# Optimization experiments

Hardware: AMD Instinct MI355X
Metric: run time of the kernel (lower is better)

Reference implementation:

```python
import jax, jax.numpy as jnp
import numpy as np

DIM = 1024
HEADS = 16
DIM_HEAD = 64
INNER = HEADS * DIM_HEAD
SCALE = DIM_HEAD ** -0.5
LN_EPS = 1e-5
MASK_VALUE = -np.finfo(np.float32).max


def setup_inputs() -> dict:
    key = jax.random.key(0)
    ks = jax.random.split(key, 3)
    x = jax.random.normal(ks[0], (2, 2048, DIM), dtype=jnp.float32)
    w_qkv = jax.random.normal(ks[1], (DIM, 3 * INNER), dtype=jnp.float32) * (DIM ** -0.5)
    w_out = jax.random.normal(ks[2], (INNER, DIM), dtype=jnp.float32) * (INNER ** -0.5)
    ln_gamma = jnp.ones((DIM,), dtype=jnp.float32)
    ln_beta = jnp.zeros((DIM,), dtype=jnp.float32)
    return {"x": x, "ln_gamma": ln_gamma, "ln_beta": ln_beta, "w_qkv": w_qkv, "w_out": w_out}


def reference(x, ln_gamma, ln_beta, w_qkv, w_out):
    b, n, _ = x.shape
    # LayerNorm
    mu = jnp.mean(x, axis=-1, keepdims=True)
    var = jnp.mean(jnp.square(x - mu), axis=-1, keepdims=True)
    xn = (x - mu) * jax.lax.rsqrt(var + LN_EPS) * ln_gamma + ln_beta
    # QKV projection, split into heads: b n (h d) -> b h n d
    qkv = xn @ w_qkv  # [b, n, 3*inner]
    q, k, v = jnp.split(qkv, 3, axis=-1)
    def to_heads(t):
        return t.reshape(b, n, HEADS, DIM_HEAD).transpose(0, 2, 1, 3)
    q, k, v = to_heads(q), to_heads(k), to_heads(v)
    # scaled scores with diagonal excluded
    dots = jnp.einsum('bhnd,bhmd->bhnm', q, k) * SCALE
    eye = jnp.eye(n, dtype=bool)
    dots = jnp.where(eye, MASK_VALUE, dots)
    attn = jax.nn.softmax(dots, axis=-1)
    out = jnp.einsum('bhnm,bhmd->bhnd', attn, v)
    out = out.transpose(0, 2, 1, 3).reshape(b, n, INNER)
    return out @ w_out
```

## Files before the change

### kernel.cpp

```cpp
#include <hip/hip_runtime.h>


#define DIMM   1024
#define NSEQ   2048
#define BATCH  2
#define HEADS  16
#define DHEAD  64
#define QKVN   3072
#define MROWS  4096

typedef float          f32x4  __attribute__((ext_vector_type(4)));
typedef __bf16         bf16x8 __attribute__((ext_vector_type(8)));
typedef __bf16         bf16x4 __attribute__((ext_vector_type(4)));
typedef unsigned short u16x8  __attribute__((ext_vector_type(8)));
typedef unsigned short u16x4  __attribute__((ext_vector_type(4)));

#define QSCALE (0.125f * 1.4426950408889634f)

#if __has_builtin(__builtin_amdgcn_exp2f)
#define EXP2(x) __builtin_amdgcn_exp2f(x)
#else
#define EXP2(x) exp2f(x)
#endif

__device__ __forceinline__ unsigned short f2bf(float f) {
  unsigned u = __builtin_bit_cast(unsigned, f);
  u += 0x7FFFu + ((u >> 16) & 1u);
  return (unsigned short)(u >> 16);
}
__device__ __forceinline__ bf16x8 as_bf(u16x8 v) { return __builtin_bit_cast(bf16x8, v); }

__device__ __forceinline__ u16x4 cvt4(f32x4 v) {
  bf16x4 b;
  b[0] = (__bf16)v[0]; b[1] = (__bf16)v[1]; b[2] = (__bf16)v[2]; b[3] = (__bf16)v[3];
  return __builtin_bit_cast(u16x4, b);
}

__device__ __forceinline__ void gl_lds16(const unsigned short* g, unsigned short* l) {
  __builtin_amdgcn_global_load_lds(
      (const __attribute__((address_space(1))) unsigned*)g,
      (__attribute__((address_space(3))) unsigned*)l, 16, 0, 0);
}

__device__ __forceinline__ bf16x8 lds_frag(const unsigned short* base, int row, int chunk) {
  return as_bf(*(const u16x8*)&base[row * 64 + ((chunk ^ (row & 7)) << 3)]);
}

__global__ __launch_bounds__(256) void transpose_bf16_kernel(
    const float* __restrict__ src, unsigned short* __restrict__ dst, int R, int C) {
  __shared__ float t[32][33];
  const int rb = blockIdx.y * 32, cb = blockIdx.x * 32;
  const int r0 = threadIdx.x >> 5;
  const int c  = threadIdx.x & 31;
#pragma unroll
  for (int i = 0; i < 4; ++i)
    t[r0 + i * 8][c] = src[(rb + r0 + i * 8) * C + cb + c];
  __syncthreads();
#pragma unroll
  for (int i = 0; i < 4; ++i)
    dst[(cb + r0 + i * 8) * R + rb + c] = f2bf(t[c][r0 + i * 8]);
}

__global__ __launch_bounds__(256) void ln_kernel(
    const float* __restrict__ x, const float* __restrict__ g,
    const float* __restrict__ be, unsigned short* __restrict__ xn) {
  const int row = blockIdx.x, tid = threadIdx.x;
  const int wave = tid >> 6, lane = tid & 63;
  const float4 v = *(const float4*)&x[row * DIMM + tid * 4];
  float s  = v.x + v.y + v.z + v.w;
  float s2 = v.x * v.x + v.y * v.y + v.z * v.z + v.w * v.w;
#pragma unroll
  for (int o = 32; o >= 1; o >>= 1) { s += __shfl_xor(s, o); s2 += __shfl_xor(s2, o); }
  __shared__ float ps[4], ps2[4];
  if (lane == 0) { ps[wave] = s; ps2[wave] = s2; }
  __syncthreads();
  s  = ps[0] + ps[1] + ps[2] + ps[3];
  s2 = ps2[0] + ps2[1] + ps2[2] + ps2[3];
  const float mu  = s * (1.0f / DIMM);
  const float var = s2 * (1.0f / DIMM) - mu * mu;
  const float rs  = rsqrtf(var + 1e-5f);
  const float4 gg = *(const float4*)&g[tid * 4];
  const float4 bb = *(const float4*)&be[tid * 4];
  u16x4 o;
  o[0] = f2bf((v.x - mu) * rs * gg.x + bb.x);
  o[1] = f2bf((v.y - mu) * rs * gg.y + bb.y);
  o[2] = f2bf((v.z - mu) * rs * gg.z + bb.z);
  o[3] = f2bf((v.w - mu) * rs * gg.w + bb.w);
  *(u16x4*)&xn[row * DIMM + tid * 4] = o;
}

template<bool SWAP>
__device__ __forceinline__ void gemm_core128(
    const unsigned short* __restrict__ A, const unsigned short* __restrict__ Bt,
    unsigned short* As, unsigned short* Bs, int bm, int bn, int tid,
    f32x4 (&acc)[4][4]) {
  const int wave = tid >> 6, lane = tid & 63;
  const int l15 = lane & 15, quad = lane >> 4;
  const int wm = wave >> 1, wn = wave & 1;
  const int lrow = lane >> 3;
  const int gcol = ((lane & 7) ^ lrow) << 3;
  const unsigned short* Ab = A  + (bm * 128 + wave * 32 + lrow) * DIMM + gcol;
  const unsigned short* Bb = Bt + (bn * 128 + wave * 32 + lrow) * DIMM + gcol;

  for (int k0 = 0; k0 < DIMM; k0 += 64) {
#pragma unroll
    for (int j = 0; j < 4; ++j) {
      gl_lds16(Ab + j * 8 * DIMM + k0, &As[(wave * 32 + j * 8) * 64]);
      gl_lds16(Bb + j * 8 * DIMM + k0, &Bs[(wave * 32 + j * 8) * 64]);
    }
    __syncthreads();
#pragma unroll
    for (int kk = 0; kk < 2; ++kk) {
      bf16x8 af[4], bfr[4];
#pragma unroll
      for (int mi = 0; mi < 4; ++mi) af[mi]  = lds_frag(As, wm * 64 + mi * 16 + l15, kk * 4 + quad);
#pragma unroll
      for (int ni = 0; ni < 4; ++ni) bfr[ni] = lds_frag(Bs, wn * 64 + ni * 16 + l15, kk * 4 + quad);
#pragma unroll
      for (int mi = 0; mi < 4; ++mi)
#pragma unroll
        for (int ni = 0; ni < 4; ++ni)
          acc[mi][ni] = SWAP
            ? __builtin_amdgcn_mfma_f32_16x16x32_bf16(bfr[ni], af[mi], acc[mi][ni], 0, 0, 0)
            : __builtin_amdgcn_mfma_f32_16x16x32_bf16(af[mi], bfr[ni], acc[mi][ni], 0, 0, 0);
    }
    __syncthreads();
  }
}

__global__ __launch_bounds__(256, 2) void gemm_qk_kernel(
    const unsigned short* __restrict__ A, const unsigned short* __restrict__ Bt,
    unsigned short* __restrict__ qb, unsigned short* __restrict__ kb) {
  __shared__ __attribute__((aligned(16))) unsigned short As[128 * 64];
  __shared__ __attribute__((aligned(16))) unsigned short Bs[128 * 64];
  const int tid = threadIdx.x;
  const int bm = blockIdx.y, bn = blockIdx.x;
  f32x4 acc[4][4] = {};
  gemm_core128<true>(A, Bt, As, Bs, bm, bn, tid, acc);

  const int lane = tid & 63, wave = tid >> 6;
  const int l15 = lane & 15, quad = lane >> 4;
  const int wm = wave >> 1, wn = wave & 1;
  const int colbase = bn * 128 + wn * 64;
  const int which = colbase >> 10;
  unsigned short* dst = which ? kb : qb;
  const float sc = which ? 1.0f : QSCALE;
#pragma unroll
  for (int mi = 0; mi < 4; ++mi) {
    const int m = bm * 128 + wm * 64 + mi * 16 + l15;
    const int bh0 = (m >> 11) * HEADS;
    const int n = m & 2047;
#pragma unroll
    for (int ni = 0; ni < 4; ++ni) {
      const int wc = (colbase & 1023) + ni * 16 + quad * 4;
      const int h = wc >> 6, dd = wc & 63;
      f32x4 v = acc[mi][ni] * sc;
      *(u16x4*)&dst[((bh0 + h) * NSEQ + n) * DHEAD + dd] = cvt4(v);
    }
  }
}

__global__ __launch_bounds__(256, 2) void gemm_v_kernel(
    const unsigned short* __restrict__ A, const unsigned short* __restrict__ Bt,
    unsigned short* __restrict__ vtb) {
  __shared__ __attribute__((aligned(16))) unsigned short As[128 * 64];
  __shared__ __attribute__((aligned(16))) unsigned short Bs[128 * 64];
  const int tid = threadIdx.x;
  const int bm = blockIdx.y, bn = blockIdx.x + 16;
  f32x4 acc[4][4] = {};
  gemm_core128<false>(A, Bt, As, Bs, bm, bn, tid, acc);

  const int lane = tid & 63, wave = tid >> 6;
  const int l15 = lane & 15, quad = lane >> 4;
  const int wm = wave >> 1, wn = wave & 1;
  const int colbase = bn * 128 + wn * 64 - 2048;
#pragma unroll
  for (int mi = 0; mi < 4; ++mi) {
    const int m0 = bm * 128 + wm * 64 + mi * 16 + quad * 4;
    const int bh0 = (m0 >> 11) * HEADS;
    const int n0 = m0 & 2047;
#pragma unroll
    for (int ni = 0; ni < 4; ++ni) {
      const int vcol = colbase + ni * 16 + l15;
      const int h = vcol >> 6, dd = vcol & 63;
      *(u16x4*)&vtb[((bh0 + h) * DHEAD + dd) * NSEQ + n0] = cvt4(acc[mi][ni]);
    }
  }
}

__global__ __launch_bounds__(256, 2) void attn_kernel(
    const unsigned short* __restrict__ qb, const unsigned short* __restrict__ kb,
    const unsigned short* __restrict__ vtb, unsigned short* __restrict__ attn_out) {
  __shared__ __attribute__((aligned(16))) unsigned short Ks[64 * 64];
  __shared__ __attribute__((aligned(16))) unsigned short Vts[64 * 64];
  __shared__ __attribute__((aligned(16))) unsigned short Ps[4][16][72];
  const int tid = threadIdx.x, wave = tid >> 6, lane = tid & 63;
  const int l15 = lane & 15, quad = lane >> 4;
  const int bh = blockIdx.x, qt = blockIdx.y;
  const int b = bh >> 4, h = bh & 15;
  const int qt64 = qt * 64;
  const int qg = qt64 + wave * 16 + l15;

  bf16x8 aq[2];
  const unsigned short* qrow = qb + (bh * NSEQ + qg) * DHEAD;
  aq[0] = as_bf(*(const u16x8*)(qrow + quad * 8));
  aq[1] = as_bf(*(const u16x8*)(qrow + 32 + quad * 8));

  float lsum = 0.f;
  f32x4 occ[4] = {};

  const int lrow = lane >> 3;
  const int gcol = ((lane & 7) ^ lrow) << 3;
  const unsigned short* Kb = kb  + (bh * NSEQ + wave * 16 + lrow) * DHEAD + gcol;
  const unsigned short* Vb = vtb + (bh * DHEAD + wave * 16 + lrow) * NSEQ + gcol;

  for (int kv = 0; kv < NSEQ; kv += 64) {
    gl_lds16(Kb + kv * DHEAD,             &Ks[(wave * 16) * 64]);
    gl_lds16(Kb + kv * DHEAD + 8 * DHEAD, &Ks[(wave * 16 + 8) * 64]);
    gl_lds16(Vb + kv,                     &Vts[(wave * 16) * 64]);
    gl_lds16(Vb + kv + 8 * NSEQ,          &Vts[(wave * 16 + 8) * 64]);
    __syncthreads();

    f32x4 scc[4];
#pragma unroll
    for (int ct = 0; ct < 4; ++ct) scc[ct] = (f32x4){-32.f, -32.f, -32.f, -32.f};
#pragma unroll
    for (int kk = 0; kk < 2; ++kk)
#pragma unroll
      for (int ct = 0; ct < 4; ++ct) {
        bf16x8 ak = lds_frag(Ks, ct * 16 + l15, kk * 4 + quad);
        scc[ct] = __builtin_amdgcn_mfma_f32_16x16x32_bf16(ak, aq[kk], scc[ct], 0, 0, 0);
      }

#pragma unroll
    for (int ct = 0; ct < 4; ++ct)
#pragma unroll
      for (int r = 0; r < 4; ++r) scc[ct][r] = EXP2(scc[ct][r]);

    if (kv == qt64) {
#pragma unroll
      for (int ct = 0; ct < 4; ++ct)
#pragma unroll
        for (int r = 0; r < 4; ++r) {
          const int kvo = ct * 16 + quad * 4 + r;
          if (kvo == wave * 16 + l15) scc[ct][r] = 0.f;
        }
    }

    f32x4 ps4 = (scc[0] + scc[1]) + (scc[2] + scc[3]);
    lsum += (ps4[0] + ps4[1]) + (ps4[2] + ps4[3]);

#pragma unroll
    for (int ct = 0; ct < 4; ++ct)
      *(u16x4*)&Ps[wave][l15][ct * 16 + quad * 4] = cvt4(scc[ct]);

#pragma unroll
    for (int kk = 0; kk < 2; ++kk) {
      bf16x8 bp = as_bf(*(const u16x8*)&Ps[wave][l15][kk * 32 + quad * 8]);
#pragma unroll
      for (int ct = 0; ct < 4; ++ct) {
        bf16x8 av = lds_frag(Vts, ct * 16 + l15, kk * 4 + quad);
        occ[ct] = __builtin_amdgcn_mfma_f32_16x16x32_bf16(av, bp, occ[ct], 0, 0, 0);
      }
    }
    __syncthreads();
  }
  lsum += __shfl_xor(lsum, 16);
  lsum += __shfl_xor(lsum, 32);
  const float rl = __builtin_amdgcn_rcpf(lsum);
#pragma unroll
  for (int ct = 0; ct < 4; ++ct) {
    f32x4 ov = occ[ct] * rl;
    *(u16x4*)&attn_out[(b * NSEQ + qg) * DIMM + h * DHEAD + ct * 16 + quad * 4] = cvt4(ov);
  }
}

__global__ __launch_bounds__(256, 2) void gemm_out_kernel(
    const unsigned short* __restrict__ A,
    const unsigned short* __restrict__ Bt,
    float* __restrict__ out) {
  __shared__ __attribute__((aligned(16))) unsigned short As[128 * 64];
  __shared__ __attribute__((aligned(16))) unsigned short Bs[128 * 64];
  const int tid = threadIdx.x;
  const int bm = blockIdx.y, bn = blockIdx.x;
  f32x4 acc[4][4] = {};
  gemm_core128<false>(A, Bt, As, Bs, bm, bn, tid, acc);

  const int lane = tid & 63, wave = tid >> 6;
  const int l15 = lane & 15, quad = lane >> 4;
  const int wm = wave >> 1, wn = wave & 1;
#pragma unroll
  for (int mi = 0; mi < 4; ++mi) {
    const int mrow = bm * 128 + wm * 64 + mi * 16 + quad * 4;
#pragma unroll
    for (int ni = 0; ni < 4; ++ni) {
      const int ncol = bn * 128 + wn * 64 + ni * 16 + l15;
#pragma unroll
      for (int r = 0; r < 4; ++r)
        out[(mrow + r) * DIMM + ncol] = acc[mi][ni][r];
    }
  }
}

extern "C" void kernel_launch(void* const* d_in, const int* in_sizes, int n_in,
                              void* d_out, int out_size, void* d_ws, size_t ws_size,
                              hipStream_t stream) {
  const float* x     = (const float*)d_in[0];
  const float* gamma = (const float*)d_in[1];
  const float* beta  = (const float*)d_in[2];
  const float* w_qkv = (const float*)d_in[3];
  const float* w_out = (const float*)d_in[4];
  float* out = (float*)d_out;

  char* ws = (char*)d_ws;
  unsigned short* xn    = (unsigned short*)(ws);
  unsigned short* wqkvT = (unsigned short*)(ws + 8388608);
  unsigned short* woutT = (unsigned short*)(ws + 14680064);
  unsigned short* qbuf  = (unsigned short*)(ws + 16777216);
  unsigned short* kbuf  = (unsigned short*)(ws + 25165824);
  unsigned short* vtbuf = (unsigned short*)(ws + 33554432);
  unsigned short* attnb = (unsigned short*)(ws + 41943040);

  transpose_bf16_kernel<<<dim3(QKVN / 32, DIMM / 32), 256, 0, stream>>>(w_qkv, wqkvT, DIMM, QKVN);
  transpose_bf16_kernel<<<dim3(DIMM / 32, DIMM / 32), 256, 0, stream>>>(w_out, woutT, DIMM, DIMM);
  ln_kernel<<<MROWS, 256, 0, stream>>>(x, gamma, beta, xn);
  gemm_qk_kernel<<<dim3(16, MROWS / 128), 256, 0, stream>>>(xn, wqkvT, qbuf, kbuf);
  gemm_v_kernel<<<dim3(8, MROWS / 128), 256, 0, stream>>>(xn, wqkvT, vtbuf);
  attn_kernel<<<dim3(BATCH * HEADS, NSEQ / 64), 256, 0, stream>>>(qbuf, kbuf, vtbuf, attnb);
  gemm_out_kernel<<<dim3(DIMM / 128, MROWS / 128), 256, 0, stream>>>(attnb, woutT, out);
}
```

Before: 203.2 us.

## Merge launches, double-buffer and widen attention q-tiles, vectorize output stores

The two weight transposes and the Q/K and V projection GEMMs are each merged into single launches, removing launch gaps and tail effects. The attention kernel now handles 128 queries per block (two 16-row subtiles per wave) and reuses each K/V fragment load across both. It also double-buffers the K/V tiles so the next tile's global-to-LDS copy overlaps compute. The output GEMM switches to the swapped MFMA operand order so it can write float4 rows instead of scalar strided stores. The costs are higher register and LDS use in attention, which may reduce occupancy, and half as many attention blocks.

```diff
diff --git a/kernel.cpp b/kernel.cpp
--- a/kernel.cpp
+++ b/kernel.cpp
@@ -46,12 +46,13 @@
   return as_bf(*(const u16x8*)&base[row * 64 + ((chunk ^ (row & 7)) << 3)]);
 }
 
-__global__ __launch_bounds__(256) void transpose_bf16_kernel(
-    const float* __restrict__ src, unsigned short* __restrict__ dst, int R, int C) {
+__device__ __forceinline__ void transpose_tile(
+    const float* __restrict__ src, unsigned short* __restrict__ dst,
+    int R, int C, int bx, int by, int tid) {
   __shared__ float t[32][33];
-  const int rb = blockIdx.y * 32, cb = blockIdx.x * 32;
-  const int r0 = threadIdx.x >> 5;
-  const int c  = threadIdx.x & 31;
+  const int rb = by * 32, cb = bx * 32;
+  const int r0 = tid >> 5;
+  const int c  = tid & 31;
 #pragma unroll
   for (int i = 0; i < 4; ++i)
     t[r0 + i * 8][c] = src[(rb + r0 + i * 8) * C + cb + c];
@@ -59,6 +60,14 @@
 #pragma unroll
   for (int i = 0; i < 4; ++i)
     dst[(cb + r0 + i * 8) * R + rb + c] = f2bf(t[c][r0 + i * 8]);
+}
+
+__global__ __launch_bounds__(256) void transpose2_kernel(
+    const float* __restrict__ w_qkv, const float* __restrict__ w_out,
+    unsigned short* __restrict__ wqkvT, unsigned short* __restrict__ woutT) {
+  const int bx = blockIdx.x;
+  if (bx < QKVN / 32) transpose_tile(w_qkv, wqkvT, DIMM, QKVN, bx, blockIdx.y, threadIdx.x);
+  else                transpose_tile(w_out, woutT, DIMM, DIMM, bx - QKVN / 32, blockIdx.y, threadIdx.x);
 }
 
 __global__ __launch_bounds__(256) void ln_kernel(
@@ -128,62 +137,52 @@
   }
 }
 
-__global__ __launch_bounds__(256, 2) void gemm_qk_kernel(
+__global__ __launch_bounds__(256, 2) void gemm_qkv_kernel(
     const unsigned short* __restrict__ A, const unsigned short* __restrict__ Bt,
-    unsigned short* __restrict__ qb, unsigned short* __restrict__ kb) {
+    unsigned short* __restrict__ qb, unsigned short* __restrict__ kb,
+    unsigned short* __restrict__ vtb) {
   __shared__ __attribute__((aligned(16))) unsigned short As[128 * 64];
   __shared__ __attribute__((aligned(16))) unsigned short Bs[128 * 64];
   const int tid = threadIdx.x;
   const int bm = blockIdx.y, bn = blockIdx.x;
-  f32x4 acc[4][4] = {};
-  gemm_core128<true>(A, Bt, As, Bs, bm, bn, tid, acc);
-
   const int lane = tid & 63, wave = tid >> 6;
   const int l15 = lane & 15, quad = lane >> 4;
   const int wm = wave >> 1, wn = wave & 1;
-  const int colbase = bn * 128 + wn * 64;
-  const int which = colbase >> 10;
-  unsigned short* dst = which ? kb : qb;
-  const float sc = which ? 1.0f : QSCALE;
-#pragma unroll
-  for (int mi = 0; mi < 4; ++mi) {
-    const int m = bm * 128 + wm * 64 + mi * 16 + l15;
-    const int bh0 = (m >> 11) * HEADS;
-    const int n = m & 2047;
-#pragma unroll
-    for (int ni = 0; ni < 4; ++ni) {
-      const int wc = (colbase & 1023) + ni * 16 + quad * 4;
-      const int h = wc >> 6, dd = wc & 63;
-      f32x4 v = acc[mi][ni] * sc;
-      *(u16x4*)&dst[((bh0 + h) * NSEQ + n) * DHEAD + dd] = cvt4(v);
-    }
-  }
-}
-
-__global__ __launch_bounds__(256, 2) void gemm_v_kernel(
-    const unsigned short* __restrict__ A, const unsigned short* __restrict__ Bt,
-    unsigned short* __restrict__ vtb) {
-  __shared__ __attribute__((aligned(16))) unsigned short As[128 * 64];
-  __shared__ __attribute__((aligned(16))) unsigned short Bs[128 * 64];
-  const int tid = threadIdx.x;
-  const int bm = blockIdx.y, bn = blockIdx.x + 16;
   f32x4 acc[4][4] = {};
-  gemm_core128<false>(A, Bt, As, Bs, bm, bn, tid, acc);
-
-  const int lane = tid & 63, wave = tid >> 6;
-  const int l15 = lane & 15, quad = lane >> 4;
-  const int wm = wave >> 1, wn = wave & 1;
-  const int colbase = bn * 128 + wn * 64 - 2048;
-#pragma unroll
-  for (int mi = 0; mi < 4; ++mi) {
-    const int m0 = bm * 128 + wm * 64 + mi * 16 + quad * 4;
-    const int bh0 = (m0 >> 11) * HEADS;
-    const int n0 = m0 & 2047;
-#pragma unroll
-    for (int ni = 0; ni < 4; ++ni) {
-      const int vcol = colbase + ni * 16 + l15;
-      const int h = vcol >> 6, dd = vcol & 63;
-      *(u16x4*)&vtb[((bh0 + h) * DHEAD + dd) * NSEQ + n0] = cvt4(acc[mi][ni]);
+
+  if (bn < 16) {
+    gemm_core128<true>(A, Bt, As, Bs, bm, bn, tid, acc);
+    const int colbase = bn * 128 + wn * 64;
+    const int which = colbase >> 10;
+    unsigned short* dst = which ? kb : qb;
+    const float sc = which ? 1.0f : QSCALE;
+#pragma unroll
+    for (int mi = 0; mi < 4; ++mi) {
+      const int m = bm * 128 + wm * 64 + mi * 16 + l15;
+      const int bh0 = (m >> 11) * HEADS;
+      const int n = m & 2047;
+#pragma unroll
+      for (int ni = 0; ni < 4; ++ni) {
+        const int wc = (colbase & 1023) + ni * 16 + quad * 4;
+        const int h = wc >> 6, dd = wc & 63;
+        f32x4 v = acc[mi][ni] * sc;
+        *(u16x4*)&dst[((bh0 + h) * NSEQ + n) * DHEAD + dd] = cvt4(v);
+      }
+    }
+  } else {
+    gemm_core128<false>(A, Bt, As, Bs, bm, bn, tid, acc);
+    const int colbase = bn * 128 + wn * 64 - 2048;
+#pragma unroll
+    for (int mi = 0; mi < 4; ++mi) {
+      const int m0 = bm * 128 + wm * 64 + mi * 16 + quad * 4;
+      const int bh0 = (m0 >> 11) * HEADS;
+      const int n0 = m0 & 2047;
+#pragma unroll
+      for (int ni = 0; ni < 4; ++ni) {
+        const int vcol = colbase + ni * 16 + l15;
+        const int h = vcol >> 6, dd = vcol & 63;
+        *(u16x4*)&vtb[((bh0 + h) * DHEAD + dd) * NSEQ + n0] = cvt4(acc[mi][ni]);
+      }
     }
   }
 }
@@ -191,87 +190,109 @@
 __global__ __launch_bounds__(256, 2) void attn_kernel(
     const unsigned short* __restrict__ qb, const unsigned short* __restrict__ kb,
     const unsigned short* __restrict__ vtb, unsigned short* __restrict__ attn_out) {
-  __shared__ __attribute__((aligned(16))) unsigned short Ks[64 * 64];
-  __shared__ __attribute__((aligned(16))) unsigned short Vts[64 * 64];
-  __shared__ __attribute__((aligned(16))) unsigned short Ps[4][16][72];
+  __shared__ __attribute__((aligned(16))) unsigned short Ks[2][64 * 64];
+  __shared__ __attribute__((aligned(16))) unsigned short Vts[2][64 * 64];
+  __shared__ __attribute__((aligned(16))) unsigned short Ps[4][2][16][72];
   const int tid = threadIdx.x, wave = tid >> 6, lane = tid & 63;
   const int l15 = lane & 15, quad = lane >> 4;
   const int bh = blockIdx.x, qt = blockIdx.y;
   const int b = bh >> 4, h = bh & 15;
-  const int qt64 = qt * 64;
-  const int qg = qt64 + wave * 16 + l15;
-
-  bf16x8 aq[2];
-  const unsigned short* qrow = qb + (bh * NSEQ + qg) * DHEAD;
-  aq[0] = as_bf(*(const u16x8*)(qrow + quad * 8));
-  aq[1] = as_bf(*(const u16x8*)(qrow + 32 + quad * 8));
-
-  float lsum = 0.f;
-  f32x4 occ[4] = {};
+  const int qbase = qt * 128 + wave * 32;
+
+  bf16x8 aq[2][2];
+#pragma unroll
+  for (int sub = 0; sub < 2; ++sub) {
+    const unsigned short* qrow = qb + (bh * NSEQ + qbase + sub * 16 + l15) * DHEAD;
+    aq[sub][0] = as_bf(*(const u16x8*)(qrow + quad * 8));
+    aq[sub][1] = as_bf(*(const u16x8*)(qrow + 32 + quad * 8));
+  }
+
+  float lsum[2] = {0.f, 0.f};
+  f32x4 occ[2][4] = {};
 
   const int lrow = lane >> 3;
   const int gcol = ((lane & 7) ^ lrow) << 3;
   const unsigned short* Kb = kb  + (bh * NSEQ + wave * 16 + lrow) * DHEAD + gcol;
   const unsigned short* Vb = vtb + (bh * DHEAD + wave * 16 + lrow) * NSEQ + gcol;
 
-  for (int kv = 0; kv < NSEQ; kv += 64) {
-    gl_lds16(Kb + kv * DHEAD,             &Ks[(wave * 16) * 64]);
-    gl_lds16(Kb + kv * DHEAD + 8 * DHEAD, &Ks[(wave * 16 + 8) * 64]);
-    gl_lds16(Vb + kv,                     &Vts[(wave * 16) * 64]);
-    gl_lds16(Vb + kv + 8 * NSEQ,          &Vts[(wave * 16 + 8) * 64]);
+  gl_lds16(Kb,             &Ks[0][(wave * 16) * 64]);
+  gl_lds16(Kb + 8 * DHEAD, &Ks[0][(wave * 16 + 8) * 64]);
+  gl_lds16(Vb,             &Vts[0][(wave * 16) * 64]);
+  gl_lds16(Vb + 8 * NSEQ,  &Vts[0][(wave * 16 + 8) * 64]);
+
+  const int diag_it = qt * 2 + (wave >> 1);
+
+  for (int it = 0; it < NSEQ / 64; ++it) {
+    const int cur = it & 1;
     __syncthreads();
-
-    f32x4 scc[4];
-#pragma unroll
-    for (int ct = 0; ct < 4; ++ct) scc[ct] = (f32x4){-32.f, -32.f, -32.f, -32.f};
+    if (it < NSEQ / 64 - 1) {
+      const unsigned short* Kn = Kb + (it + 1) * 64 * DHEAD;
+      const unsigned short* Vn = Vb + (it + 1) * 64;
+      gl_lds16(Kn,             &Ks[cur ^ 1][(wave * 16) * 64]);
+      gl_lds16(Kn + 8 * DHEAD, &Ks[cur ^ 1][(wave * 16 + 8) * 64]);
+      gl_lds16(Vn,             &Vts[cur ^ 1][(wave * 16) * 64]);
+      gl_lds16(Vn + 8 * NSEQ,  &Vts[cur ^ 1][(wave * 16 + 8) * 64]);
+    }
+    bf16x8 ak[2][4], av[2][4];
 #pragma unroll
     for (int kk = 0; kk < 2; ++kk)
 #pragma unroll
       for (int ct = 0; ct < 4; ++ct) {
-        bf16x8 ak = lds_frag(Ks, ct * 16 + l15, kk * 4 + quad);
-        scc[ct] = __builtin_amdgcn_mfma_f32_16x16x32_bf16(ak, aq[kk], scc[ct], 0, 0, 0);
-      }
-
-#pragma unroll
-    for (int ct = 0; ct < 4; ++ct)
-#pragma unroll
-      for (int r = 0; r < 4; ++r) scc[ct][r] = EXP2(scc[ct][r]);
-
-    if (kv == qt64) {
+        ak[kk][ct] = lds_frag(&Ks[cur][0],  ct * 16 + l15, kk * 4 + quad);
+        av[kk][ct] = lds_frag(&Vts[cur][0], ct * 16 + l15, kk * 4 + quad);
+      }
+#pragma unroll
+    for (int sub = 0; sub < 2; ++sub) {
+      f32x4 scc[4];
+#pragma unroll
+      for (int ct = 0; ct < 4; ++ct) scc[ct] = (f32x4){-32.f, -32.f, -32.f, -32.f};
+#pragma unroll
+      for (int kk = 0; kk < 2; ++kk)
+#pragma unroll
+        for (int ct = 0; ct < 4; ++ct)
+          scc[ct] = __builtin_amdgcn_mfma_f32_16x16x32_bf16(ak[kk][ct], aq[sub][kk], scc[ct], 0, 0, 0);
 #pragma unroll
       for (int ct = 0; ct < 4; ++ct)
 #pragma unroll
-        for (int r = 0; r < 4; ++r) {
-          const int kvo = ct * 16 + quad * 4 + r;
-          if (kvo == wave * 16 + l15) scc[ct][r] = 0.f;
-        }
-    }
-
-    f32x4 ps4 = (scc[0] + scc[1]) + (scc[2] + scc[3]);
-    lsum += (ps4[0] + ps4[1]) + (ps4[2] + ps4[3]);
-
-#pragma unroll
-    for (int ct = 0; ct < 4; ++ct)
-      *(u16x4*)&Ps[wave][l15][ct * 16 + quad * 4] = cvt4(scc[ct]);
-
-#pragma unroll
-    for (int kk = 0; kk < 2; ++kk) {
-      bf16x8 bp = as_bf(*(const u16x8*)&Ps[wave][l15][kk * 32 + quad * 8]);
-#pragma unroll
-      for (int ct = 0; ct < 4; ++ct) {
-        bf16x8 av = lds_frag(Vts, ct * 16 + l15, kk * 4 + quad);
-        occ[ct] = __builtin_amdgcn_mfma_f32_16x16x32_bf16(av, bp, occ[ct], 0, 0, 0);
-      }
-    }
-    __syncthreads();
-  }
-  lsum += __shfl_xor(lsum, 16);
-  lsum += __shfl_xor(lsum, 32);
-  const float rl = __builtin_amdgcn_rcpf(lsum);
-#pragma unroll
-  for (int ct = 0; ct < 4; ++ct) {
-    f32x4 ov = occ[ct] * rl;
-    *(u16x4*)&attn_out[(b * NSEQ + qg) * DIMM + h * DHEAD + ct * 16 + quad * 4] = cvt4(ov);
+        for (int r = 0; r < 4; ++r) scc[ct][r] = EXP2(scc[ct][r]);
+
+      if (it == diag_it) {
+        const int kvo_want = (wave & 1) * 32 + sub * 16 + l15;
+#pragma unroll
+        for (int ct = 0; ct < 4; ++ct)
+#pragma unroll
+          for (int r = 0; r < 4; ++r)
+            if (ct * 16 + quad * 4 + r == kvo_want) scc[ct][r] = 0.f;
+      }
+
+      f32x4 ps4 = (scc[0] + scc[1]) + (scc[2] + scc[3]);
+      lsum[sub] += (ps4[0] + ps4[1]) + (ps4[2] + ps4[3]);
+
+#pragma unroll
+      for (int ct = 0; ct < 4; ++ct)
+        *(u16x4*)&Ps[wave][sub][l15][ct * 16 + quad * 4] = cvt4(scc[ct]);
+
+#pragma unroll
+      for (int kk = 0; kk < 2; ++kk) {
+        bf16x8 bp = as_bf(*(const u16x8*)&Ps[wave][sub][l15][kk * 32 + quad * 8]);
+#pragma unroll
+        for (int ct = 0; ct < 4; ++ct)
+          occ[sub][ct] = __builtin_amdgcn_mfma_f32_16x16x32_bf16(av[kk][ct], bp, occ[sub][ct], 0, 0, 0);
+      }
+    }
+  }
+#pragma unroll
+  for (int sub = 0; sub < 2; ++sub) {
+    float l = lsum[sub];
+    l += __shfl_xor(l, 16);
+    l += __shfl_xor(l, 32);
+    const float rl = __builtin_amdgcn_rcpf(l);
+    const int qg = qbase + sub * 16 + l15;
+#pragma unroll
+    for (int ct = 0; ct < 4; ++ct) {
+      f32x4 ov = occ[sub][ct] * rl;
+      *(u16x4*)&attn_out[(b * NSEQ + qg) * DIMM + h * DHEAD + ct * 16 + quad * 4] = cvt4(ov);
+    }
   }
 }
 
@@ -284,20 +305,18 @@
   const int tid = threadIdx.x;
   const int bm = blockIdx.y, bn = blockIdx.x;
   f32x4 acc[4][4] = {};
-  gemm_core128<false>(A, Bt, As, Bs, bm, bn, tid, acc);
+  gemm_core128<true>(A, Bt, As, Bs, bm, bn, tid, acc);
 
   const int lane = tid & 63, wave = tid >> 6;
   const int l15 = lane & 15, quad = lane >> 4;
   const int wm = wave >> 1, wn = wave & 1;
 #pragma unroll
   for (int mi = 0; mi < 4; ++mi) {
-    const int mrow = bm * 128 + wm * 64 + mi * 16 + quad * 4;
+    const int m = bm * 128 + wm * 64 + mi * 16 + l15;
 #pragma unroll
     for (int ni = 0; ni < 4; ++ni) {
-      const int ncol = bn * 128 + wn * 64 + ni * 16 + l15;
-#pragma unroll
-      for (int r = 0; r < 4; ++r)
-        out[(mrow + r) * DIMM + ncol] = acc[mi][ni][r];
+      const int col = bn * 128 + wn * 64 + ni * 16 + quad * 4;
+      *(f32x4*)&out[m * DIMM + col] = acc[mi][ni];
     }
   }
 }
@@ -321,11 +340,9 @@
   unsigned short* vtbuf = (unsigned short*)(ws + 33554432);
   unsigned short* attnb = (unsigned short*)(ws + 41943040);
 
-  transpose_bf16_kernel<<<dim3(QKVN / 32, DIMM / 32), 256, 0, stream>>>(w_qkv, wqkvT, DIMM, QKVN);
-  transpose_bf16_kernel<<<dim3(DIMM / 32, DIMM / 32), 256, 0, stream>>>(w_out, woutT, DIMM, DIMM);
+  transpose2_kernel<<<dim3((QKVN + DIMM) / 32, DIMM / 32), 256, 0, stream>>>(w_qkv, w_out, wqkvT, woutT);
   ln_kernel<<<MROWS, 256, 0, stream>>>(x, gamma, beta, xn);
-  gemm_qk_kernel<<<dim3(16, MROWS / 128), 256, 0, stream>>>(xn, wqkvT, qbuf, kbuf);
-  gemm_v_kernel<<<dim3(8, MROWS / 128), 256, 0, stream>>>(xn, wqkvT, vtbuf);
-  attn_kernel<<<dim3(BATCH * HEADS, NSEQ / 64), 256, 0, stream>>>(qbuf, kbuf, vtbuf, attnb);
+  gemm_qkv_kernel<<<dim3(24, MROWS / 128), 256, 0, stream>>>(xn, wqkvT, qbuf, kbuf, vtbuf);
+  attn_kernel<<<dim3(BATCH * HEADS, NSEQ / 128), 256, 0, stream>>>(qbuf, kbuf, vtbuf, attnb);
   gemm_out_kernel<<<dim3(DIMM / 128, MROWS / 128), 256, 0, stream>>>(attnb, woutT, out);
 }
```

Measured after the change: 189.3 us. 1.07x faster.
